# Kernel tuning notes

Measured on AMD Instinct MI355X. Metric: run time of the kernel, lower is better.

Reference implementation:

```python
import jax, jax.numpy as jnp
import numpy as np

B, N, E = 2, 10000, 160000
NODE_DIM, EDGE_DIM, HIDDEN = 128, 64, 256


def setup_inputs() -> dict:
    key = jax.random.key(0)
    ks = jax.random.split(key, 12)
    def lin(k, fan_in, fan_out):
        return jax.random.normal(k, (fan_in, fan_out), dtype=jnp.float32) / np.sqrt(fan_in)
    msg_in = 2 * NODE_DIM + EDGE_DIM   # 320
    upd_in = NODE_DIM + HIDDEN         # 384
    return {
        "node_features": jax.random.normal(ks[0], (B, N, NODE_DIM), dtype=jnp.float32),
        "edge_indices": jax.random.randint(ks[1], (B, E, 2), 0, N, dtype=jnp.int32),
        "edge_features": jax.random.normal(ks[2], (B, E, EDGE_DIM), dtype=jnp.float32),
        "W1m": lin(ks[3], msg_in, HIDDEN),  "b1m": jnp.zeros((HIDDEN,), jnp.float32),
        "W2m": lin(ks[4], HIDDEN, HIDDEN),  "b2m": jnp.zeros((HIDDEN,), jnp.float32),
        "W1u": lin(ks[5], upd_in, HIDDEN),  "b1u": jnp.zeros((HIDDEN,), jnp.float32),
        "W2u": lin(ks[6], HIDDEN, NODE_DIM), "b2u": jnp.zeros((NODE_DIM,), jnp.float32),
    }


def reference(node_features, edge_indices, edge_features,
              W1m, b1m, W2m, b2m, W1u, b1u, W2u, b2u):
    # node_features: [B, N, D]; edge_indices: [B, E, 2]; edge_features: [B, E, F]
    b, n, d = node_features.shape
    e = edge_indices.shape[1]
    src_idx = edge_indices[..., 0]  # [B, E]
    dst_idx = edge_indices[..., 1]  # [B, E]
    # batched gather of endpoint features
    src = jnp.take_along_axis(node_features, src_idx[..., None], axis=1)  # [B, E, D]
    dst = jnp.take_along_axis(node_features, dst_idx[..., None], axis=1)  # [B, E, D]
    msg_in = jnp.concatenate([src, dst, edge_features], axis=-1)          # [B, E, 2D+F]
    h = jax.nn.gelu(jnp.einsum("bei,ih->beh", msg_in, W1m) + b1m)
    messages = jnp.einsum("beh,ho->beo", h, W2m) + b2m                    # [B, E, H]
    # scatter-add into destination node buckets (flatten batch for segment_sum)
    flat_dst = (dst_idx + (jnp.arange(b, dtype=dst_idx.dtype)[:, None] * n)).reshape(-1)
    aggregated = jax.ops.segment_sum(
        messages.reshape(b * e, -1), flat_dst, num_segments=b * n
    ).reshape(b, n, -1)                                                   # [B, N, H]
    upd_in = jnp.concatenate([node_features, aggregated], axis=-1)        # [B, N, D+H]
    u = jax.nn.gelu(jnp.einsum("bni,ih->bnh", upd_in, W1u) + b1u)
    return jnp.einsum("bnh,ho->bno", u, W2u) + b2u                        # [B, N, D]
```

## Files before the change

kernel.cpp:

```cpp
#include <hip/hip_runtime.h>
#include <hip/hip_bf16.h>
#include <math.h>

#define BATCH   2
#define N_NODES 10000
#define E_EDGES 160000
#define BN      (BATCH * N_NODES)
#define BE      (BATCH * E_EDGES)
#define ND      128
#define ED      64
#define HID     256
#define K1      320
#define K2      256
#define K1U     384
#define NOUT    128
#define TM      64
#define TME     64
#define LDH     264
#define SCAN_BLOCKS ((BN + 1023) / 1024)

typedef __attribute__((ext_vector_type(8))) short bf16x8;
typedef __attribute__((ext_vector_type(4))) float f32x4;

__device__ float          g_P[(size_t)BN * 512];
__device__ unsigned short g_nodef_bf[(size_t)BN * ND];
__device__ unsigned short g_w1c[HID * K1U];
__device__ unsigned short g_w2ut[K2 * NOUT];
__device__ float          g_bc[HID];
__device__ int            g_hist[BN];

__device__ __forceinline__ float gelu_tanh(float x) {
    float u = 0.7978845608028654f * (x + 0.044715f * x * x * x);
    float e = __expf(2.0f * u);
    float t = 1.0f - 2.0f * __builtin_amdgcn_rcpf(e + 1.0f);
    return 0.5f * x * (1.0f + t);
}

__device__ __forceinline__ unsigned short f2bf(float f) {
    __hip_bfloat16 h = __float2bfloat16(f);
    return *reinterpret_cast<unsigned short*>(&h);
}

__device__ __forceinline__ float bf2f(unsigned short u) {
    unsigned int x = ((unsigned int)u) << 16;
    return *reinterpret_cast<float*>(&x);
}


__global__ __launch_bounds__(256) void f32_to_bf16_vec(
    const float* __restrict__ in, int n4)
{
    int i = blockIdx.x * blockDim.x + threadIdx.x;
    if (i < n4) {
        float4 v = ((const float4*)in)[i];
        ushort4 o;
        o.x = f2bf(v.x); o.y = f2bf(v.y); o.z = f2bf(v.z); o.w = f2bf(v.w);
        ((ushort4*)g_nodef_bf)[i] = o;
    }
    if (i < BN) g_hist[i] = 0;
}

__global__ __launch_bounds__(256) void prep_weights(
    const float* __restrict__ W1m, unsigned short* __restrict__ w1t,
    const float* __restrict__ W1u, const float* __restrict__ W2u)
{
    int id = blockIdx.x * blockDim.x + threadIdx.x;
    if (id < K1 * HID) {
        int k = id % K1, n = id / K1;
        w1t[id] = f2bf(W1m[(size_t)k * HID + n]);
    }
    if (id < ND * HID) {
        int k = id % ND, n = id / ND;
        g_w1c[n * K1U + k] = f2bf(W1u[(size_t)k * HID + n]);
    }
    if (id < K2 * NOUT) {
        int k = id % K2, n = id / K2;
        g_w2ut[id] = f2bf(W2u[(size_t)k * NOUT + n]);
    }
}

__global__ __launch_bounds__(256) void prep_wc(
    const float* __restrict__ W2m, const float* __restrict__ W1u,
    const float* __restrict__ b2m)
{
    int t = blockIdx.x * blockDim.x + threadIdx.x;
    int n = t & 255;
    int j = t >> 8;
    float a = 0.f;
    for (int o = 0; o < HID; ++o)
        a += W2m[(size_t)j * HID + o] * W1u[(size_t)(128 + o) * HID + n];
    g_w1c[n * K1U + 128 + j] = f2bf(a);
    if (t < HID) {
        float c = 0.f;
        for (int o = 0; o < HID; ++o)
            c += b2m[o] * W1u[(size_t)(128 + o) * HID + t];
        g_bc[t] = c;
    }
}

__global__ __launch_bounds__(256) void dst_hist(const int* __restrict__ eidx)
{
    int e = blockIdx.x * blockDim.x + threadIdx.x;
    if (e < BE) {
        int dst = eidx[2 * e + 1];
        int b   = e / E_EDGES;
        atomicAdd(&g_hist[b * N_NODES + dst], 1);
    }
}


__global__ __launch_bounds__(1024) void scan_partial(
    int* __restrict__ offs, int* __restrict__ bsum)
{
    __shared__ int buf[1024];
    int tid = threadIdx.x;
    int i   = blockIdx.x * 1024 + tid;
    int v   = (i < BN) ? g_hist[i] : 0;
    buf[tid] = v;
    __syncthreads();
    #pragma unroll
    for (int d = 1; d < 1024; d <<= 1) {
        int t = (tid >= d) ? buf[tid - d] : 0;
        __syncthreads();
        buf[tid] += t;
        __syncthreads();
    }
    int incl = buf[tid];
    if (i < BN) offs[i] = incl - v;
    if (tid == 1023) bsum[blockIdx.x] = incl;
}

__global__ __launch_bounds__(1024) void scan_add(
    int* __restrict__ offs, const int* __restrict__ bsum)
{
    __shared__ int sbase;
    int tid = threadIdx.x;
    if (tid < 64) {
        int v = (tid < blockIdx.x && tid < SCAN_BLOCKS) ? bsum[tid] : 0;
        #pragma unroll
        for (int d = 32; d > 0; d >>= 1) v += __shfl_down(v, d);
        if (tid == 0) sbase = v;
    }
    __syncthreads();
    int i = blockIdx.x * 1024 + tid;
    if (i < BN) offs[i] += sbase;
}

__global__ __launch_bounds__(256) void dst_scatter(
    const int* __restrict__ eidx, int* __restrict__ offs, int* __restrict__ perm)
{
    int e = blockIdx.x * blockDim.x + threadIdx.x;
    if (e < BE) {
        int dst  = eidx[2 * e + 1];
        int b    = e / E_EDGES;
        int pos  = atomicAdd(&offs[b * N_NODES + dst], 1);
        perm[pos] = e;
    }
}

__global__ __launch_bounds__(512, 2) void pgemm(const unsigned short* __restrict__ w1t)
{
    const int tid  = threadIdx.x;
    const int wave = tid >> 6;
    const int lane = tid & 63;
    const int quad = lane >> 4;
    const int r16  = lane & 15;
    const int n0   = blockIdx.x * TM;

    const int jb   = (wave & 3) * 64;
    const int koff = (wave < 4) ? 0 : 128;
    const int cb   = (wave < 4) ? 0 : 256;

    f32x4 acc[4][4];
    #pragma unroll
    for (int mt = 0; mt < 4; ++mt)
        #pragma unroll
        for (int nt = 0; nt < 4; ++nt)
            acc[mt][nt] = (f32x4){0.f, 0.f, 0.f, 0.f};

    for (int ks = 0; ks < ND / 32; ++ks) {
        bf16x8 wf[4], nf[4];
        #pragma unroll
        for (int nt = 0; nt < 4; ++nt)
            wf[nt] = *(const bf16x8*)&w1t[(size_t)(jb + nt * 16 + r16) * K1
                                          + koff + ks * 32 + quad * 8];
        #pragma unroll
        for (int mt = 0; mt < 4; ++mt) {
            int row = n0 + mt * 16 + r16; if (row >= BN) row = BN - 1;
            nf[mt] = *(const bf16x8*)&g_nodef_bf[(size_t)row * ND + ks * 32 + quad * 8];
        }
        #pragma unroll
        for (int mt = 0; mt < 4; ++mt)
            #pragma unroll
            for (int nt = 0; nt < 4; ++nt)
                acc[mt][nt] = __builtin_amdgcn_mfma_f32_16x16x32_bf16(
                    wf[nt], nf[mt], acc[mt][nt], 0, 0, 0);
    }

    #pragma unroll
    for (int nt = 0; nt < 4; ++nt) {
        int j0 = cb + jb + nt * 16 + quad * 4;
        #pragma unroll
        for (int mt = 0; mt < 4; ++mt) {
            int m = n0 + mt * 16 + r16;
            if (m < BN) {
                float4 v = {acc[mt][nt][0], acc[mt][nt][1],
                            acc[mt][nt][2], acc[mt][nt][3]};
                *(float4*)&g_P[(size_t)m * 512 + j0] = v;
            }
        }
    }
}

#define EK_SE   0
#define EK_SH   8192
#define EK_SMEM (8192 + TME * LDH * 2)

__global__ __launch_bounds__(512, 6) void edge_mlp_mfma(
    const int*            __restrict__ eidx,
    const float*          __restrict__ edgef,
    const int*            __restrict__ perm,
    const unsigned short* __restrict__ w1t,
    const float*          __restrict__ b1m,
    float* __restrict__ agg)
{
    __shared__ __align__(16) char smem[EK_SMEM];
    unsigned short* sE = (unsigned short*)(smem + EK_SE);
    unsigned short* sH = (unsigned short*)(smem + EK_SH);
    __shared__ int s_src[TME];
    __shared__ int s_dst[TME];
    __shared__ int s_eid[TME];

    const int tid  = threadIdx.x;
    const int wave = tid >> 6;
    const int lane = tid & 63;
    const int quad = lane >> 4;
    const int r16  = lane & 15;
    const int be0  = blockIdx.x * TME;

    if (tid < TME) {
        int eid = perm[be0 + tid];
        int b   = eid / E_EDGES;
        int2 se = ((const int2*)eidx)[eid];
        s_eid[tid] = eid;
        s_src[tid] = b * N_NODES + se.x;
        s_dst[tid] = b * N_NODES + se.y;
    }

    const unsigned short* wB1 = w1t + (size_t)(wave * 32) * K1 + 256;
    bf16x8 wf00 = *(const bf16x8*)&wB1[(size_t)r16        * K1 + quad * 8];
    bf16x8 wf01 = *(const bf16x8*)&wB1[(size_t)r16        * K1 + 32 + quad * 8];
    bf16x8 wf10 = *(const bf16x8*)&wB1[(size_t)(16 + r16) * K1 + quad * 8];
    bf16x8 wf11 = *(const bf16x8*)&wB1[(size_t)(16 + r16) * K1 + 32 + quad * 8];

    __syncthreads();

    {
        int row = tid >> 3;
        int c0  = (tid & 7) * 8;
        const float* fp = edgef + (size_t)s_eid[row] * ED + c0;
        float4 v0 = *(const float4*)fp;
        float4 v1 = *(const float4*)(fp + 4);
        ushort4 o0, o1;
        o0.x = f2bf(v0.x); o0.y = f2bf(v0.y); o0.z = f2bf(v0.z); o0.w = f2bf(v0.w);
        o1.x = f2bf(v1.x); o1.y = f2bf(v1.y); o1.z = f2bf(v1.z); o1.w = f2bf(v1.w);
        int p2 = c0 >> 5, kk = c0 & 31;
        *(ushort4*)&sE[p2 * 2048 + row * 32 + kk]     = o0;
        *(ushort4*)&sE[p2 * 2048 + row * 32 + kk + 4] = o1;
    }
    __syncthreads();

    f32x4 acc[4][2];
    #pragma unroll
    for (int mt = 0; mt < 4; ++mt)
        #pragma unroll
        for (int nt = 0; nt < 2; ++nt)
            acc[mt][nt] = (f32x4){0.f, 0.f, 0.f, 0.f};

    #pragma unroll
    for (int mt = 0; mt < 4; ++mt) {
        bf16x8 e0 = *(const bf16x8*)&sE[(mt * 16 + r16) * 32 + quad * 8];
        bf16x8 e1 = *(const bf16x8*)&sE[2048 + (mt * 16 + r16) * 32 + quad * 8];
        acc[mt][0] = __builtin_amdgcn_mfma_f32_16x16x32_bf16(wf00, e0, acc[mt][0], 0, 0, 0);
        acc[mt][1] = __builtin_amdgcn_mfma_f32_16x16x32_bf16(wf10, e0, acc[mt][1], 0, 0, 0);
        acc[mt][0] = __builtin_amdgcn_mfma_f32_16x16x32_bf16(wf01, e1, acc[mt][0], 0, 0, 0);
        acc[mt][1] = __builtin_amdgcn_mfma_f32_16x16x32_bf16(wf11, e1, acc[mt][1], 0, 0, 0);
    }

    {
        float4 bb[2];
        bb[0] = *(const float4*)&b1m[wave * 32 + quad * 4];
        bb[1] = *(const float4*)&b1m[wave * 32 + 16 + quad * 4];
        #pragma unroll
        for (int mt = 0; mt < 4; ++mt) {
            int m = mt * 16 + r16;
            const float* pS = &g_P[(size_t)s_src[m] * 512];
            const float* pD = &g_P[(size_t)s_dst[m] * 512 + 256];
            #pragma unroll
            for (int nt = 0; nt < 2; ++nt) {
                int n0 = wave * 32 + nt * 16 + quad * 4;
                float4 vs = *(const float4*)(pS + n0);
                float4 vd = *(const float4*)(pD + n0);
                ushort4 o;
                o.x = f2bf(gelu_tanh(acc[mt][nt][0] + vs.x + vd.x + bb[nt].x));
                o.y = f2bf(gelu_tanh(acc[mt][nt][1] + vs.y + vd.y + bb[nt].y));
                o.z = f2bf(gelu_tanh(acc[mt][nt][2] + vs.z + vd.z + bb[nt].z));
                o.w = f2bf(gelu_tanh(acc[mt][nt][3] + vs.w + vd.w + bb[nt].w));
                *(ushort4*)&sH[m * LDH + n0] = o;
            }
        }
    }
    __syncthreads();

    {
        const int cc = tid & 255;
        const int r0 = (tid >> 8) * 32;
        int   cur  = s_dst[r0];
        float racc = 0.f;
        for (int mb = 0; mb < 32; mb += 8) {
            float v[8];
            #pragma unroll
            for (int j = 0; j < 8; ++j)
                v[j] = bf2f(sH[(r0 + mb + j) * LDH + cc]);
            #pragma unroll
            for (int j = 0; j < 8; ++j) {
                int d = s_dst[r0 + mb + j];
                if (d != cur) {
                    atomicAdd(&agg[(size_t)cur * HID + cc], racc);
                    cur = d; racc = v[j];
                } else {
                    racc += v[j];
                }
            }
        }
        atomicAdd(&agg[(size_t)cur * HID + cc], racc);
    }
}

__global__ __launch_bounds__(256, 4) void node_mlp_mfma(
    const float* __restrict__ agg,
    const float* __restrict__ b1u,
    const float* __restrict__ b2u,
    float* __restrict__ out)
{
    __shared__ __align__(16) unsigned short sH[TM * LDH];

    const int tid  = threadIdx.x;
    const int wave = tid >> 6;
    const int lane = tid & 63;
    const int quad = lane >> 4;
    const int r16  = lane & 15;
    const int n0   = blockIdx.x * TM;

    f32x4 acc[4][4];
    #pragma unroll
    for (int mt = 0; mt < 4; ++mt)
        #pragma unroll
        for (int nt = 0; nt < 4; ++nt)
            acc[mt][nt] = (f32x4){0.f, 0.f, 0.f, 0.f};

    for (int ks = 0; ks < 4; ++ks) {
        bf16x8 wf[4], nf[4];
        #pragma unroll
        for (int nt = 0; nt < 4; ++nt)
            wf[nt] = *(const bf16x8*)&g_w1c[(size_t)(wave * 64 + nt * 16 + r16) * K1U
                                            + ks * 32 + quad * 8];
        #pragma unroll
        for (int mt = 0; mt < 4; ++mt) {
            int row = n0 + mt * 16 + r16; if (row >= BN) row = BN - 1;
            nf[mt] = *(const bf16x8*)&g_nodef_bf[(size_t)row * ND + ks * 32 + quad * 8];
        }
        #pragma unroll
        for (int mt = 0; mt < 4; ++mt)
            #pragma unroll
            for (int nt = 0; nt < 4; ++nt)
                acc[mt][nt] = __builtin_amdgcn_mfma_f32_16x16x32_bf16(
                    wf[nt], nf[mt], acc[mt][nt], 0, 0, 0);
    }
    for (int ks = 0; ks < 8; ++ks) {
        bf16x8 wf[4], nf[4];
        #pragma unroll
        for (int nt = 0; nt < 4; ++nt)
            wf[nt] = *(const bf16x8*)&g_w1c[(size_t)(wave * 64 + nt * 16 + r16) * K1U
                                            + (4 + ks) * 32 + quad * 8];
        #pragma unroll
        for (int mt = 0; mt < 4; ++mt) {
            int row = n0 + mt * 16 + r16; if (row >= BN) row = BN - 1;
            const float* fp = &agg[(size_t)row * HID + ks * 32 + quad * 8];
            float4 v0 = *(const float4*)fp;
            float4 v1 = *(const float4*)(fp + 4);
            union { bf16x8 v; ushort4 u[2]; } cv;
            cv.u[0] = (ushort4){f2bf(v0.x), f2bf(v0.y), f2bf(v0.z), f2bf(v0.w)};
            cv.u[1] = (ushort4){f2bf(v1.x), f2bf(v1.y), f2bf(v1.z), f2bf(v1.w)};
            nf[mt] = cv.v;
        }
        #pragma unroll
        for (int mt = 0; mt < 4; ++mt)
            #pragma unroll
            for (int nt = 0; nt < 4; ++nt)
                acc[mt][nt] = __builtin_amdgcn_mfma_f32_16x16x32_bf16(
                    wf[nt], nf[mt], acc[mt][nt], 0, 0, 0);
    }

    #pragma unroll
    for (int nt = 0; nt < 4; ++nt) {
        int nn0 = wave * 64 + nt * 16 + quad * 4;
        float4 bb = *(const float4*)&b1u[nn0];
        float4 bc = *(const float4*)&g_bc[nn0];
        #pragma unroll
        for (int mt = 0; mt < 4; ++mt) {
            int row = n0 + mt * 16 + r16; if (row >= BN) row = BN - 1;
            float hv = (float)g_hist[row];
            int m = mt * 16 + r16;
            ushort4 o;
            o.x = f2bf(gelu_tanh(acc[mt][nt][0] + bb.x + hv * bc.x));
            o.y = f2bf(gelu_tanh(acc[mt][nt][1] + bb.y + hv * bc.y));
            o.z = f2bf(gelu_tanh(acc[mt][nt][2] + bb.z + hv * bc.z));
            o.w = f2bf(gelu_tanh(acc[mt][nt][3] + bb.w + hv * bc.w));
            *(ushort4*)&sH[m * LDH + nn0] = o;
        }
    }
    __syncthreads();

    f32x4 acc2[4][2];
    #pragma unroll
    for (int mt = 0; mt < 4; ++mt)
        #pragma unroll
        for (int nt = 0; nt < 2; ++nt)
            acc2[mt][nt] = (f32x4){0.f, 0.f, 0.f, 0.f};

    for (int ks = 0; ks < K2 / 32; ++ks) {
        bf16x8 wf2[2], hf[4];
        #pragma unroll
        for (int nt = 0; nt < 2; ++nt)
            wf2[nt] = *(const bf16x8*)&g_w2ut[(size_t)(wave * 32 + nt * 16 + r16) * K2
                                              + ks * 32 + quad * 8];
        #pragma unroll
        for (int mt = 0; mt < 4; ++mt)
            hf[mt] = *(const bf16x8*)&sH[(mt * 16 + r16) * LDH + ks * 32 + quad * 8];
        #pragma unroll
        for (int mt = 0; mt < 4; ++mt)
            #pragma unroll
            for (int nt = 0; nt < 2; ++nt)
                acc2[mt][nt] = __builtin_amdgcn_mfma_f32_16x16x32_bf16(
                    wf2[nt], hf[mt], acc2[mt][nt], 0, 0, 0);
    }

    #pragma unroll
    for (int nt = 0; nt < 2; ++nt) {
        int j0 = wave * 32 + nt * 16 + quad * 4;
        float4 bb = *(const float4*)&b2u[j0];
        #pragma unroll
        for (int mt = 0; mt < 4; ++mt) {
            int row = n0 + mt * 16 + r16;
            if (row < BN) {
                float4 v = {acc2[mt][nt][0] + bb.x, acc2[mt][nt][1] + bb.y,
                            acc2[mt][nt][2] + bb.z, acc2[mt][nt][3] + bb.w};
                *(float4*)&out[(size_t)row * NOUT + j0] = v;
            }
        }
    }
}


extern "C" void kernel_launch(void* const* d_in, const int* in_sizes, int n_in,
                              void* d_out, int out_size, void* d_ws, size_t ws_size,
                              hipStream_t stream) {
    const float* nodef = (const float*)d_in[0];
    const int*   eidx  = (const int*)  d_in[1];
    const float* edgef = (const float*)d_in[2];
    const float* W1m   = (const float*)d_in[3];
    const float* b1m   = (const float*)d_in[4];
    const float* W2m   = (const float*)d_in[5];
    const float* b2m   = (const float*)d_in[6];
    const float* W1u   = (const float*)d_in[7];
    const float* b1u   = (const float*)d_in[8];
    const float* W2u   = (const float*)d_in[9];
    const float* b2u   = (const float*)d_in[10];
    float* out = (float*)d_out;

    char* wsb = (char*)d_ws;
    float* agg = (float*)wsb;
    const size_t AGG_B = (size_t)BN * HID * sizeof(float);

    char* ob = (char*)d_out;
    unsigned short* w1t  = (unsigned short*)(ob + 5120000);
    int* offs            = (int*)(ob + 5494912);
    int* perm            = (int*)(ob + 5574912);
    int* bsum            = (int*)(ob + 6854912);

    hipMemsetAsync(agg, 0, AGG_B, stream);

    {
        int n4 = BN * ND / 4;
        f32_to_bf16_vec<<<(n4 + 255) / 256, 256, 0, stream>>>(nodef, n4);
    }
    prep_weights<<<(K1 * HID + 255) / 256, 256, 0, stream>>>(W1m, w1t, W1u, W2u);
    prep_wc<<<(HID * HID) / 256, 256, 0, stream>>>(W2m, W1u, b2m);

    pgemm<<<(BN + TM - 1) / TM, 512, 0, stream>>>(w1t);

    dst_hist<<<(BE + 255) / 256, 256, 0, stream>>>(eidx);
    scan_partial<<<SCAN_BLOCKS, 1024, 0, stream>>>(offs, bsum);
    scan_add<<<SCAN_BLOCKS, 1024, 0, stream>>>(offs, bsum);
    dst_scatter<<<(BE + 255) / 256, 256, 0, stream>>>(eidx, offs, perm);

    edge_mlp_mfma<<<BE / TME, 512, 0, stream>>>(
        eidx, edgef, perm, w1t, b1m, agg);

    node_mlp_mfma<<<(BN + TM - 1) / TM, 256, 0, stream>>>(agg, b1u, b2u, out);
}
```

Baseline: 365.5 us.

## Store node projections in bf16, merge prep kernels, single-block scan, widen node MLP

The per-node projection buffer P is now stored as bf16 instead of fp32, which halves the random gather traffic in the edge MLP at some cost in precision. The three weight and feature prep kernels are merged into one launch, and the two-kernel scan becomes a single 1024-thread block that scans 20 elements per thread. The node MLP moves from 256 to 512 threads per block, so each wave covers half as many output columns. Together these cut launch count and memory traffic, but they add bf16 rounding of the projection and make the scan a single serial block.

```diff
diff --git a/kernel.cpp b/kernel.cpp
--- a/kernel.cpp
+++ b/kernel.cpp
@@ -17,12 +17,11 @@
 #define TM      64
 #define TME     64
 #define LDH     264
-#define SCAN_BLOCKS ((BN + 1023) / 1024)
 
 typedef __attribute__((ext_vector_type(8))) short bf16x8;
 typedef __attribute__((ext_vector_type(4))) float f32x4;
 
-__device__ float          g_P[(size_t)BN * 512];
+__device__ unsigned short g_Pb[(size_t)BN * 512];
 __device__ unsigned short g_nodef_bf[(size_t)BN * ND];
 __device__ unsigned short g_w1c[HID * K1U];
 __device__ unsigned short g_w2ut[K2 * NOUT];
@@ -46,55 +45,47 @@
     return *reinterpret_cast<float*>(&x);
 }
 
-
-__global__ __launch_bounds__(256) void f32_to_bf16_vec(
-    const float* __restrict__ in, int n4)
+__global__ __launch_bounds__(256) void prep_all(
+    const float* __restrict__ nodef,
+    const float* __restrict__ W1m, unsigned short* __restrict__ w1t,
+    const float* __restrict__ W1u, const float* __restrict__ W2u,
+    const float* __restrict__ W2m, const float* __restrict__ b2m)
 {
     int i = blockIdx.x * blockDim.x + threadIdx.x;
-    if (i < n4) {
-        float4 v = ((const float4*)in)[i];
+    if (i < BN * ND / 4) {
+        float4 v = ((const float4*)nodef)[i];
         ushort4 o;
         o.x = f2bf(v.x); o.y = f2bf(v.y); o.z = f2bf(v.z); o.w = f2bf(v.w);
         ((ushort4*)g_nodef_bf)[i] = o;
     }
     if (i < BN) g_hist[i] = 0;
-}
-
-__global__ __launch_bounds__(256) void prep_weights(
-    const float* __restrict__ W1m, unsigned short* __restrict__ w1t,
-    const float* __restrict__ W1u, const float* __restrict__ W2u)
-{
-    int id = blockIdx.x * blockDim.x + threadIdx.x;
-    if (id < K1 * HID) {
-        int k = id % K1, n = id / K1;
-        w1t[id] = f2bf(W1m[(size_t)k * HID + n]);
-    }
-    if (id < ND * HID) {
-        int k = id % ND, n = id / ND;
+    if (i < K1 * HID) {
+        int k = i % K1, n = i / K1;
+        w1t[i] = f2bf(W1m[(size_t)k * HID + n]);
+    }
+    if (i < ND * HID) {
+        int k = i % ND, n = i / ND;
         g_w1c[n * K1U + k] = f2bf(W1u[(size_t)k * HID + n]);
     }
-    if (id < K2 * NOUT) {
-        int k = id % K2, n = id / K2;
-        g_w2ut[id] = f2bf(W2u[(size_t)k * NOUT + n]);
-    }
-}
-
-__global__ __launch_bounds__(256) void prep_wc(
-    const float* __restrict__ W2m, const float* __restrict__ W1u,
-    const float* __restrict__ b2m)
-{
-    int t = blockIdx.x * blockDim.x + threadIdx.x;
-    int n = t & 255;
-    int j = t >> 8;
-    float a = 0.f;
-    for (int o = 0; o < HID; ++o)
-        a += W2m[(size_t)j * HID + o] * W1u[(size_t)(128 + o) * HID + n];
-    g_w1c[n * K1U + 128 + j] = f2bf(a);
-    if (t < HID) {
+    if (i < K2 * NOUT) {
+        int k = i % K2, n = i / K2;
+        g_w2ut[i] = f2bf(W2u[(size_t)k * NOUT + n]);
+    }
+    if (i < HID * HID) {
+        int n = i & 255;
+        int j = i >> 8;
+        float a = 0.f;
+        #pragma unroll 8
+        for (int o = 0; o < HID; ++o)
+            a += W2m[(size_t)j * HID + o] * W1u[(size_t)(128 + o) * HID + n];
+        g_w1c[n * K1U + 128 + j] = f2bf(a);
+    }
+    if (i < HID) {
         float c = 0.f;
+        #pragma unroll 8
         for (int o = 0; o < HID; ++o)
-            c += b2m[o] * W1u[(size_t)(128 + o) * HID + t];
-        g_bc[t] = c;
+            c += b2m[o] * W1u[(size_t)(128 + o) * HID + i];
+        g_bc[i] = c;
     }
 }
 
@@ -108,42 +99,34 @@
     }
 }
 
-
-__global__ __launch_bounds__(1024) void scan_partial(
-    int* __restrict__ offs, int* __restrict__ bsum)
-{
-    __shared__ int buf[1024];
-    int tid = threadIdx.x;
-    int i   = blockIdx.x * 1024 + tid;
-    int v   = (i < BN) ? g_hist[i] : 0;
-    buf[tid] = v;
+__global__ __launch_bounds__(1024, 1) void scan20k(int* __restrict__ offs)
+{
+    __shared__ int tots[1024];
+    const int tid  = threadIdx.x;
+    const int base = tid * 20;
+    int v[20];
+    int s = 0;
+    #pragma unroll
+    for (int j = 0; j < 20; ++j) {
+        int i = base + j;
+        int h = (i < BN) ? g_hist[i] : 0;
+        v[j] = s; s += h;
+    }
+    tots[tid] = s;
     __syncthreads();
     #pragma unroll
     for (int d = 1; d < 1024; d <<= 1) {
-        int t = (tid >= d) ? buf[tid - d] : 0;
+        int t = (tid >= d) ? tots[tid - d] : 0;
         __syncthreads();
-        buf[tid] += t;
+        tots[tid] += t;
         __syncthreads();
     }
-    int incl = buf[tid];
-    if (i < BN) offs[i] = incl - v;
-    if (tid == 1023) bsum[blockIdx.x] = incl;
-}
-
-__global__ __launch_bounds__(1024) void scan_add(
-    int* __restrict__ offs, const int* __restrict__ bsum)
-{
-    __shared__ int sbase;
-    int tid = threadIdx.x;
-    if (tid < 64) {
-        int v = (tid < blockIdx.x && tid < SCAN_BLOCKS) ? bsum[tid] : 0;
-        #pragma unroll
-        for (int d = 32; d > 0; d >>= 1) v += __shfl_down(v, d);
-        if (tid == 0) sbase = v;
-    }
-    __syncthreads();
-    int i = blockIdx.x * 1024 + tid;
-    if (i < BN) offs[i] += sbase;
+    int excl = tots[tid] - s;
+    #pragma unroll
+    for (int j = 0; j < 20; ++j) {
+        int i = base + j;
+        if (i < BN) offs[i] = excl + v[j];
+    }
 }
 
 __global__ __launch_bounds__(256) void dst_scatter(
@@ -204,9 +187,10 @@
         for (int mt = 0; mt < 4; ++mt) {
             int m = n0 + mt * 16 + r16;
             if (m < BN) {
-                float4 v = {acc[mt][nt][0], acc[mt][nt][1],
-                            acc[mt][nt][2], acc[mt][nt][3]};
-                *(float4*)&g_P[(size_t)m * 512 + j0] = v;
+                ushort4 o;
+                o.x = f2bf(acc[mt][nt][0]); o.y = f2bf(acc[mt][nt][1]);
+                o.z = f2bf(acc[mt][nt][2]); o.w = f2bf(acc[mt][nt][3]);
+                *(ushort4*)&g_Pb[(size_t)m * 512 + j0] = o;
             }
         }
     }
@@ -294,18 +278,18 @@
         #pragma unroll
         for (int mt = 0; mt < 4; ++mt) {
             int m = mt * 16 + r16;
-            const float* pS = &g_P[(size_t)s_src[m] * 512];
-            const float* pD = &g_P[(size_t)s_dst[m] * 512 + 256];
+            const unsigned short* pS = &g_Pb[(size_t)s_src[m] * 512];
+            const unsigned short* pD = &g_Pb[(size_t)s_dst[m] * 512 + 256];
             #pragma unroll
             for (int nt = 0; nt < 2; ++nt) {
                 int n0 = wave * 32 + nt * 16 + quad * 4;
-                float4 vs = *(const float4*)(pS + n0);
-                float4 vd = *(const float4*)(pD + n0);
+                ushort4 us = *(const ushort4*)(pS + n0);
+                ushort4 ud = *(const ushort4*)(pD + n0);
                 ushort4 o;
-                o.x = f2bf(gelu_tanh(acc[mt][nt][0] + vs.x + vd.x + bb[nt].x));
-                o.y = f2bf(gelu_tanh(acc[mt][nt][1] + vs.y + vd.y + bb[nt].y));
-                o.z = f2bf(gelu_tanh(acc[mt][nt][2] + vs.z + vd.z + bb[nt].z));
-                o.w = f2bf(gelu_tanh(acc[mt][nt][3] + vs.w + vd.w + bb[nt].w));
+                o.x = f2bf(gelu_tanh(acc[mt][nt][0] + bf2f(us.x) + bf2f(ud.x) + bb[nt].x));
+                o.y = f2bf(gelu_tanh(acc[mt][nt][1] + bf2f(us.y) + bf2f(ud.y) + bb[nt].y));
+                o.z = f2bf(gelu_tanh(acc[mt][nt][2] + bf2f(us.z) + bf2f(ud.z) + bb[nt].z));
+                o.w = f2bf(gelu_tanh(acc[mt][nt][3] + bf2f(us.w) + bf2f(ud.w) + bb[nt].w));
                 *(ushort4*)&sH[m * LDH + n0] = o;
             }
         }
@@ -337,7 +321,7 @@
     }
 }
 
-__global__ __launch_bounds__(256, 4) void node_mlp_mfma(
+__global__ __launch_bounds__(512, 2) void node_mlp_mfma(
     const float* __restrict__ agg,
     const float* __restrict__ b1u,
     const float* __restrict__ b2u,
@@ -352,18 +336,18 @@
     const int r16  = lane & 15;
     const int n0   = blockIdx.x * TM;
 
-    f32x4 acc[4][4];
+    f32x4 acc[4][2];
     #pragma unroll
     for (int mt = 0; mt < 4; ++mt)
         #pragma unroll
-        for (int nt = 0; nt < 4; ++nt)
+        for (int nt = 0; nt < 2; ++nt)
             acc[mt][nt] = (f32x4){0.f, 0.f, 0.f, 0.f};
 
     for (int ks = 0; ks < 4; ++ks) {
-        bf16x8 wf[4], nf[4];
-        #pragma unroll
-        for (int nt = 0; nt < 4; ++nt)
-            wf[nt] = *(const bf16x8*)&g_w1c[(size_t)(wave * 64 + nt * 16 + r16) * K1U
+        bf16x8 wf[2], nf[4];
+        #pragma unroll
+        for (int nt = 0; nt < 2; ++nt)
+            wf[nt] = *(const bf16x8*)&g_w1c[(size_t)(wave * 32 + nt * 16 + r16) * K1U
                                             + ks * 32 + quad * 8];
         #pragma unroll
         for (int mt = 0; mt < 4; ++mt) {
@@ -373,15 +357,15 @@
         #pragma unroll
         for (int mt = 0; mt < 4; ++mt)
             #pragma unroll
-            for (int nt = 0; nt < 4; ++nt)
+            for (int nt = 0; nt < 2; ++nt)
                 acc[mt][nt] = __builtin_amdgcn_mfma_f32_16x16x32_bf16(
                     wf[nt], nf[mt], acc[mt][nt], 0, 0, 0);
     }
     for (int ks = 0; ks < 8; ++ks) {
-        bf16x8 wf[4], nf[4];
-        #pragma unroll
-        for (int nt = 0; nt < 4; ++nt)
-            wf[nt] = *(const bf16x8*)&g_w1c[(size_t)(wave * 64 + nt * 16 + r16) * K1U
+        bf16x8 wf[2], nf[4];
+        #pragma unroll
+        for (int nt = 0; nt < 2; ++nt)
+            wf[nt] = *(const bf16x8*)&g_w1c[(size_t)(wave * 32 + nt * 16 + r16) * K1U
                                             + (4 + ks) * 32 + quad * 8];
         #pragma unroll
         for (int mt = 0; mt < 4; ++mt) {
@@ -397,14 +381,14 @@
         #pragma unroll
         for (int mt = 0; mt < 4; ++mt)
             #pragma unroll
-            for (int nt = 0; nt < 4; ++nt)
+            for (int nt = 0; nt < 2; ++nt)
                 acc[mt][nt] = __builtin_amdgcn_mfma_f32_16x16x32_bf16(
                     wf[nt], nf[mt], acc[mt][nt], 0, 0, 0);
     }
 
     #pragma unroll
-    for (int nt = 0; nt < 4; ++nt) {
-        int nn0 = wave * 64 + nt * 16 + quad * 4;
+    for (int nt = 0; nt < 2; ++nt) {
+        int nn0 = wave * 32 + nt * 16 + quad * 4;
         float4 bb = *(const float4*)&b1u[nn0];
         float4 bc = *(const float4*)&g_bc[nn0];
         #pragma unroll
@@ -422,40 +406,33 @@
     }
     __syncthreads();
 
-    f32x4 acc2[4][2];
+    f32x4 acc2[4];
     #pragma unroll
     for (int mt = 0; mt < 4; ++mt)
-        #pragma unroll
-        for (int nt = 0; nt < 2; ++nt)
-            acc2[mt][nt] = (f32x4){0.f, 0.f, 0.f, 0.f};
+        acc2[mt] = (f32x4){0.f, 0.f, 0.f, 0.f};
 
     for (int ks = 0; ks < K2 / 32; ++ks) {
-        bf16x8 wf2[2], hf[4];
-        #pragma unroll
-        for (int nt = 0; nt < 2; ++nt)
-            wf2[nt] = *(const bf16x8*)&g_w2ut[(size_t)(wave * 32 + nt * 16 + r16) * K2
-                                              + ks * 32 + quad * 8];
+        bf16x8 wf2, hf[4];
+        wf2 = *(const bf16x8*)&g_w2ut[(size_t)(wave * 16 + r16) * K2
+                                      + ks * 32 + quad * 8];
         #pragma unroll
         for (int mt = 0; mt < 4; ++mt)
             hf[mt] = *(const bf16x8*)&sH[(mt * 16 + r16) * LDH + ks * 32 + quad * 8];
         #pragma unroll
         for (int mt = 0; mt < 4; ++mt)
-            #pragma unroll
-            for (int nt = 0; nt < 2; ++nt)
-                acc2[mt][nt] = __builtin_amdgcn_mfma_f32_16x16x32_bf16(
-                    wf2[nt], hf[mt], acc2[mt][nt], 0, 0, 0);
-    }
-
-    #pragma unroll
-    for (int nt = 0; nt < 2; ++nt) {
-        int j0 = wave * 32 + nt * 16 + quad * 4;
+            acc2[mt] = __builtin_amdgcn_mfma_f32_16x16x32_bf16(
+                wf2, hf[mt], acc2[mt], 0, 0, 0);
+    }
+
+    {
+        int j0 = wave * 16 + quad * 4;
         float4 bb = *(const float4*)&b2u[j0];
         #pragma unroll
         for (int mt = 0; mt < 4; ++mt) {
             int row = n0 + mt * 16 + r16;
             if (row < BN) {
-                float4 v = {acc2[mt][nt][0] + bb.x, acc2[mt][nt][1] + bb.y,
-                            acc2[mt][nt][2] + bb.z, acc2[mt][nt][3] + bb.w};
+                float4 v = {acc2[mt][0] + bb.x, acc2[mt][1] + bb.y,
+                            acc2[mt][2] + bb.z, acc2[mt][3] + bb.w};
                 *(float4*)&out[(size_t)row * NOUT + j0] = v;
             }
         }
@@ -487,26 +464,20 @@
     unsigned short* w1t  = (unsigned short*)(ob + 5120000);
     int* offs            = (int*)(ob + 5494912);
     int* perm            = (int*)(ob + 5574912);
-    int* bsum            = (int*)(ob + 6854912);
 
     hipMemsetAsync(agg, 0, AGG_B, stream);
 
-    {
-        int n4 = BN * ND / 4;
-        f32_to_bf16_vec<<<(n4 + 255) / 256, 256, 0, stream>>>(nodef, n4);
-    }
-    prep_weights<<<(K1 * HID + 255) / 256, 256, 0, stream>>>(W1m, w1t, W1u, W2u);
-    prep_wc<<<(HID * HID) / 256, 256, 0, stream>>>(W2m, W1u, b2m);
+    prep_all<<<(BN * ND / 4 + 255) / 256, 256, 0, stream>>>(
+        nodef, W1m, w1t, W1u, W2u, W2m, b2m);
+
+    dst_hist<<<(BE + 255) / 256, 256, 0, stream>>>(eidx);
+    scan20k<<<1, 1024, 0, stream>>>(offs);
+    dst_scatter<<<(BE + 255) / 256, 256, 0, stream>>>(eidx, offs, perm);
 
     pgemm<<<(BN + TM - 1) / TM, 512, 0, stream>>>(w1t);
-
-    dst_hist<<<(BE + 255) / 256, 256, 0, stream>>>(eidx);
-    scan_partial<<<SCAN_BLOCKS, 1024, 0, stream>>>(offs, bsum);
-    scan_add<<<SCAN_BLOCKS, 1024, 0, stream>>>(offs, bsum);
-    dst_scatter<<<(BE + 255) / 256, 256, 0, stream>>>(eidx, offs, perm);
 
     edge_mlp_mfma<<<BE / TME, 512, 0, stream>>>(
         eidx, edgef, perm, w1t, b1m, agg);
 
-    node_mlp_mfma<<<(BN + TM - 1) / TM, 256, 0, stream>>>(agg, b1u, b2u, out);
-}
+    node_mlp_mfma<<<(BN + TM - 1) / TM, 512, 0, stream>>>(agg, b1u, b2u, out);
+}
```

After: 380.6 us. 4.1% more time.
